# Kernel tuning notes

Hardware: AMD Instinct MI355X
Metric: run time of the kernel (lower is better)

The kernel has to match this reference:

```python
import jax, jax.numpy as jnp
import numpy as np

IN_FEATURES = 4096
LOCAL_FEATURES = 128
KERNEL_SIZE = 64
STRIDE = 32
FOLD_NUM = (IN_FEATURES - KERNEL_SIZE) // STRIDE + 1  # 127
BATCH = 4096


def setup_inputs() -> dict:
    key = jax.random.key(0)
    kx, kw, kb = jax.random.split(key, 3)
    x = jax.random.normal(kx, (BATCH, IN_FEATURES), dtype=jnp.float32)
    # Per-window linear weights: torch Linear weight is [out, in] = [local_features, kernel_size]
    bound = 1.0 / np.sqrt(KERNEL_SIZE)
    W = jax.random.uniform(kw, (FOLD_NUM, LOCAL_FEATURES, KERNEL_SIZE),
                           dtype=jnp.float32, minval=-bound, maxval=bound)
    b = jax.random.uniform(kb, (FOLD_NUM, LOCAL_FEATURES),
                           dtype=jnp.float32, minval=-bound, maxval=bound)
    return {"x": x, "W": W, "b": b}


def reference(x, W, b) -> jnp.ndarray:
    # Unfold: windows[f, k] = x[:, f*stride + k] -> [B, FOLD_NUM, KERNEL_SIZE]
    idx = jnp.arange(FOLD_NUM)[:, None] * STRIDE + jnp.arange(KERNEL_SIZE)[None, :]
    windows = x[:, idx]  # [B, F, K]
    # Batched per-window linear: out[b, f, l] = sum_k windows[b,f,k] * W[f,l,k] + b[f,l]
    out = jnp.einsum('bfk,flk->bfl', windows, W) + b[None, :, :]
    # torch.cat along dim 1 over fold index == reshape [B, F*L]
    return out.reshape(x.shape[0], FOLD_NUM * LOCAL_FEATURES)
```

## Files before the change

kernel.cpp:

```cpp
#include <hip/hip_runtime.h>
#include <hip/hip_bf16.h>

#define IN_F 4096
#define LOCAL_F 128
#define KSZ 64
#define STRIDE_ 32
#define FOLDS 127
#define BATCH_ 4096
#define OUT_F (FOLDS * LOCAL_F)

#define BM 64
#define NF 4
#define XCOLS (NF * STRIDE_ + (KSZ - STRIDE_))
#define LDSP 168

typedef __attribute__((ext_vector_type(8))) short bf16x8;
typedef __attribute__((ext_vector_type(4))) float f32x4;

__device__ __forceinline__ unsigned short f2bf(float f) {
    unsigned u = __builtin_bit_cast(unsigned, f);
    u += 0x7fffu + ((u >> 16) & 1u);
    return (unsigned short)(u >> 16);
}

__global__ __launch_bounds__(256, 2)
void local_linear_kernel(const float* __restrict__ x,
                         const float* __restrict__ W,
                         const float* __restrict__ b,
                         float* __restrict__ out) {
    __shared__ unsigned short xs[BM][LDSP];

    const int bg = blockIdx.x;
    const int fg = blockIdx.y;
    const int row0 = bg * BM;
    const int col0 = fg * (NF * STRIDE_);

    const int t = threadIdx.x;

    #pragma unroll
    for (int it = 0; it < (BM * (XCOLS / 4)) / 256; ++it) {
        int i  = t + it * 256;
        int r  = i / (XCOLS / 4);
        int c4 = i - r * (XCOLS / 4);
        int gcol = col0 + c4 * 4;
        float4 v = make_float4(0.f, 0.f, 0.f, 0.f);
        if (gcol < IN_F) {
            v = *reinterpret_cast<const float4*>(x + (size_t)(row0 + r) * IN_F + gcol);
        }
        ushort4 s;
        s.x = f2bf(v.x); s.y = f2bf(v.y); s.z = f2bf(v.z); s.w = f2bf(v.w);
        *reinterpret_cast<ushort4*>(&xs[r][c4 * 4]) = s;
    }
    __syncthreads();

    const int wave = t >> 6;
    const int lane = t & 63;
    const int f = fg * NF + wave;
    if (f >= FOLDS) return;

    const int l16 = lane & 15;
    const int g   = lane >> 4;

    f32x4 acc[4][8];
    #pragma unroll
    for (int mt = 0; mt < 4; ++mt)
        #pragma unroll
        for (int nt = 0; nt < 8; ++nt)
            acc[mt][nt] = (f32x4){0.f, 0.f, 0.f, 0.f};

    const float* Wf = W + (size_t)f * (LOCAL_F * KSZ);
    const int fcol = wave * STRIDE_;

    #pragma unroll
    for (int ks = 0; ks < 2; ++ks) {
        bf16x8 wf[8];
        #pragma unroll
        for (int nt = 0; nt < 8; ++nt) {
            const float* p = Wf + (nt * 16 + l16) * KSZ + ks * 32 + g * 8;
            float4 va = *reinterpret_cast<const float4*>(p);
            float4 vb = *reinterpret_cast<const float4*>(p + 4);
            bf16x8 w8;
            w8[0] = (short)f2bf(va.x); w8[1] = (short)f2bf(va.y);
            w8[2] = (short)f2bf(va.z); w8[3] = (short)f2bf(va.w);
            w8[4] = (short)f2bf(vb.x); w8[5] = (short)f2bf(vb.y);
            w8[6] = (short)f2bf(vb.z); w8[7] = (short)f2bf(vb.w);
            wf[nt] = w8;
        }
        bf16x8 af[4];
        #pragma unroll
        for (int mt = 0; mt < 4; ++mt) {
            af[mt] = *reinterpret_cast<const bf16x8*>(&xs[mt * 16 + l16][fcol + ks * 32 + g * 8]);
        }
        #pragma unroll
        for (int mt = 0; mt < 4; ++mt)
            #pragma unroll
            for (int nt = 0; nt < 8; ++nt)
                acc[mt][nt] = __builtin_amdgcn_mfma_f32_16x16x32_bf16(af[mt], wf[nt], acc[mt][nt], 0, 0, 0);
    }

    #pragma unroll
    for (int nt = 0; nt < 8; ++nt) {
        const int gcol = f * LOCAL_F + nt * 16 + l16;
        const float bv = b[f * LOCAL_F + nt * 16 + l16];
        #pragma unroll
        for (int mt = 0; mt < 4; ++mt) {
            #pragma unroll
            for (int j = 0; j < 4; ++j) {
                const int grow = row0 + mt * 16 + g * 4 + j;
                out[(size_t)grow * OUT_F + gcol] = acc[mt][nt][j] + bv;
            }
        }
    }
}

extern "C" void kernel_launch(void* const* d_in, const int* in_sizes, int n_in,
                              void* d_out, int out_size, void* d_ws, size_t ws_size,
                              hipStream_t stream) {
    const float* x = (const float*)d_in[0];
    const float* W = (const float*)d_in[1];
    const float* b = (const float*)d_in[2];
    float* out = (float*)d_out;
    dim3 grid(BATCH_ / BM, (FOLDS + NF - 1) / NF);
    local_linear_kernel<<<grid, 256, 0, stream>>>(x, W, b, out);
}
```

Measured before the change: 123.2 us.

## Pre-convert weights to bf16 and swap MFMA operands for vectorized output stores

Result: faster. 117.7 us (-4.5%).

```diff
diff --git a/kernel.cpp b/kernel.cpp
--- a/kernel.cpp
+++ b/kernel.cpp
@@ -8,6 +8,7 @@
 #define FOLDS 127
 #define BATCH_ 4096
 #define OUT_F (FOLDS * LOCAL_F)
+#define WN (FOLDS * LOCAL_F * KSZ)
 
 #define BM 64
 #define NF 4
@@ -15,6 +16,7 @@
 #define LDSP 168
 
 typedef __attribute__((ext_vector_type(8))) short bf16x8;
+typedef __attribute__((ext_vector_type(8))) unsigned short u16x8;
 typedef __attribute__((ext_vector_type(4))) float f32x4;
 
 __device__ __forceinline__ unsigned short f2bf(float f) {
@@ -23,9 +25,23 @@
     return (unsigned short)(u >> 16);
 }
 
+__global__ __launch_bounds__(256)
+void wprep_kernel(const float* __restrict__ W, unsigned short* __restrict__ Wbf) {
+    int i = (blockIdx.x * 256 + threadIdx.x) * 8;
+    if (i >= WN) return;
+    float4 a = *reinterpret_cast<const float4*>(W + i);
+    float4 c = *reinterpret_cast<const float4*>(W + i + 4);
+    u16x8 s;
+    s[0] = f2bf(a.x); s[1] = f2bf(a.y); s[2] = f2bf(a.z); s[3] = f2bf(a.w);
+    s[4] = f2bf(c.x); s[5] = f2bf(c.y); s[6] = f2bf(c.z); s[7] = f2bf(c.w);
+    *reinterpret_cast<u16x8*>(Wbf + i) = s;
+}
+
+template<bool WB>
 __global__ __launch_bounds__(256, 2)
 void local_linear_kernel(const float* __restrict__ x,
-                         const float* __restrict__ W,
+                         const float* __restrict__ Wf32,
+                         const unsigned short* __restrict__ Wbf,
                          const float* __restrict__ b,
                          float* __restrict__ out) {
     __shared__ unsigned short xs[BM][LDSP];
@@ -68,7 +84,6 @@
         for (int nt = 0; nt < 8; ++nt)
             acc[mt][nt] = (f32x4){0.f, 0.f, 0.f, 0.f};
 
-    const float* Wf = W + (size_t)f * (LOCAL_F * KSZ);
     const int fcol = wave * STRIDE_;
 
     #pragma unroll
@@ -76,15 +91,20 @@
         bf16x8 wf[8];
         #pragma unroll
         for (int nt = 0; nt < 8; ++nt) {
-            const float* p = Wf + (nt * 16 + l16) * KSZ + ks * 32 + g * 8;
-            float4 va = *reinterpret_cast<const float4*>(p);
-            float4 vb = *reinterpret_cast<const float4*>(p + 4);
-            bf16x8 w8;
-            w8[0] = (short)f2bf(va.x); w8[1] = (short)f2bf(va.y);
-            w8[2] = (short)f2bf(va.z); w8[3] = (short)f2bf(va.w);
-            w8[4] = (short)f2bf(vb.x); w8[5] = (short)f2bf(vb.y);
-            w8[6] = (short)f2bf(vb.z); w8[7] = (short)f2bf(vb.w);
-            wf[nt] = w8;
+            if (WB) {
+                wf[nt] = *reinterpret_cast<const bf16x8*>(
+                    Wbf + ((size_t)f * LOCAL_F + nt * 16 + l16) * KSZ + ks * 32 + g * 8);
+            } else {
+                const float* p = Wf32 + ((size_t)f * LOCAL_F + nt * 16 + l16) * KSZ + ks * 32 + g * 8;
+                float4 va = *reinterpret_cast<const float4*>(p);
+                float4 vb = *reinterpret_cast<const float4*>(p + 4);
+                bf16x8 w8;
+                w8[0] = (short)f2bf(va.x); w8[1] = (short)f2bf(va.y);
+                w8[2] = (short)f2bf(va.z); w8[3] = (short)f2bf(va.w);
+                w8[4] = (short)f2bf(vb.x); w8[5] = (short)f2bf(vb.y);
+                w8[6] = (short)f2bf(vb.z); w8[7] = (short)f2bf(vb.w);
+                wf[nt] = w8;
+            }
         }
         bf16x8 af[4];
         #pragma unroll
@@ -95,20 +115,21 @@
         for (int mt = 0; mt < 4; ++mt)
             #pragma unroll
             for (int nt = 0; nt < 8; ++nt)
-                acc[mt][nt] = __builtin_amdgcn_mfma_f32_16x16x32_bf16(af[mt], wf[nt], acc[mt][nt], 0, 0, 0);
+                acc[mt][nt] = __builtin_amdgcn_mfma_f32_16x16x32_bf16(wf[nt], af[mt], acc[mt][nt], 0, 0, 0);
     }
 
+    f32x4 bv[8];
     #pragma unroll
-    for (int nt = 0; nt < 8; ++nt) {
-        const int gcol = f * LOCAL_F + nt * 16 + l16;
-        const float bv = b[f * LOCAL_F + nt * 16 + l16];
+    for (int nt = 0; nt < 8; ++nt)
+        bv[nt] = *reinterpret_cast<const f32x4*>(b + (size_t)f * LOCAL_F + nt * 16 + 4 * g);
+
+    #pragma unroll
+    for (int mt = 0; mt < 4; ++mt) {
+        float* orow = out + (size_t)(row0 + mt * 16 + l16) * OUT_F + f * LOCAL_F + 4 * g;
         #pragma unroll
-        for (int mt = 0; mt < 4; ++mt) {
-            #pragma unroll
-            for (int j = 0; j < 4; ++j) {
-                const int grow = row0 + mt * 16 + g * 4 + j;
-                out[(size_t)grow * OUT_F + gcol] = acc[mt][nt][j] + bv;
-            }
+        for (int nt = 0; nt < 8; ++nt) {
+            f32x4 v = acc[mt][nt] + bv[nt];
+            *reinterpret_cast<f32x4*>(orow + nt * 16) = v;
         }
     }
 }
@@ -121,5 +142,12 @@
     const float* b = (const float*)d_in[2];
     float* out = (float*)d_out;
     dim3 grid(BATCH_ / BM, (FOLDS + NF - 1) / NF);
-    local_linear_kernel<<<grid, 256, 0, stream>>>(x, W, b, out);
+
+    if (ws_size >= (size_t)WN * sizeof(unsigned short)) {
+        unsigned short* Wbf = (unsigned short*)d_ws;
+        wprep_kernel<<<(WN / 8 + 255) / 256, 256, 0, stream>>>(W, Wbf);
+        local_linear_kernel<true><<<grid, 256, 0, stream>>>(x, W, Wbf, b, out);
+    } else {
+        local_linear_kernel<false><<<grid, 256, 0, stream>>>(x, W, nullptr, b, out);
+    }
 }
```
